# Performance work log

Hardware: AMD Instinct MI355X
Metric: run time of the kernel (lower is better)

Reference implementation:

```python
import jax, jax.numpy as jnp
import numpy as np

N_NODES = 100000
N_EDGES = 1600000
D_FEAT = 64
K = 5


def setup_inputs() -> dict:
    key = jax.random.key(0)
    k1, k2, k3 = jax.random.split(key, 3)
    feat = jax.random.normal(k1, (N_NODES, D_FEAT), dtype=jnp.float32)
    theta = jnp.asarray([1.0, -0.8, 0.45, -0.2, 0.08], dtype=jnp.float32)
    src = jax.random.randint(k2, (N_EDGES,), 0, N_NODES, dtype=jnp.int32)
    dst = jax.random.randint(k3, (N_EDGES,), 0, N_NODES, dtype=jnp.int32)
    return {"feat": feat, "theta": theta, "src": src, "dst": dst}


def reference(feat, theta, src, dst):
    n = feat.shape[0]
    # in-degrees: number of edges terminating at each node, clamped to >= 1
    deg = jax.ops.segment_sum(jnp.ones_like(dst, dtype=feat.dtype), dst, num_segments=n)
    d_invsqrt = jnp.maximum(deg, 1.0) ** -0.5  # [N]
    d_invsqrt = d_invsqrt[:, None]  # [N, 1]

    def unn_laplacian(x):
        scaled = x * d_invsqrt  # [N, D]
        agg = jax.ops.segment_sum(scaled[src], dst, num_segments=n)  # [N, D]
        return x - agg * d_invsqrt

    h = theta[0] * feat
    for k in range(1, theta.shape[0]):
        feat = unn_laplacian(feat)
        h = h + theta[k] * feat
    return h
```

## Files before the change

### kernel.cpp

```cpp
#include <hip/hip_runtime.h>
#include <hip/hip_bf16.h>
#include <hip/hip_fp16.h>

#define WG 256
#define WGB 1024
#define D 64
#define MAXNB 1024

__device__ inline float ld_mixed(const void* p, int bf, long i) {
    if (bf) {
        unsigned short u = ((const unsigned short*)p)[i];
        return __uint_as_float(((unsigned int)u) << 16);
    }
    return ((const float*)p)[i];
}


__global__ __launch_bounds__(WGB) void kc_hist(
        const int* __restrict__ dst, int E, int NBc, int CPB,
        int* __restrict__ histmat,
        const void* __restrict__ theta, int* __restrict__ flag) {
    __shared__ int h[MAXNB];
    int B = blockIdx.x, t = threadIdx.x;
    if (B == 0 && t == 0) {
        unsigned int w = *(const unsigned int*)theta;
        *flag = (w == 0x3F800000u) ? 0 : 1;
    }
    for (int i = t; i < NBc; i += WGB) h[i] = 0;
    __syncthreads();
    int base = B * CPB;
    int end = min(base + CPB, E);
    for (int e = base + t; e < end; e += WGB)
        atomicAdd(&h[dst[e] >> 8], 1);
    __syncthreads();
    for (int i = t; i < NBc; i += WGB)
        histmat[(long)i * NBc + B] = h[i];
}

__global__ void k_scan1(const int* __restrict__ in, int M,
                        int* __restrict__ out, int* __restrict__ part) {
    __shared__ int s[WG];
    int g = blockIdx.x * WG + threadIdx.x;
    int t = threadIdx.x;
    int v0 = (g < M) ? in[g] : 0;
    s[t] = v0;
    __syncthreads();
    for (int o = 1; o < WG; o <<= 1) {
        int v = (t >= o) ? s[t - o] : 0;
        __syncthreads();
        s[t] += v;
        __syncthreads();
    }
    if (g < M) out[g] = s[t] - v0;
    if (t == WG - 1) part[blockIdx.x] = s[t];
}

__global__ __launch_bounds__(WGB) void kc_scatter(
        const int* __restrict__ src, const int* __restrict__ dst, int E,
        int NBc, int CPB, const int* __restrict__ outx,
        const int* __restrict__ part, int P,
        unsigned int* __restrict__ tmp) {
    __shared__ int off[MAXNB];
    __shared__ int ps[1024];
    __shared__ int pex[1024];
    int B = blockIdx.x, t = threadIdx.x;
    int pv = (t < P) ? part[t] : 0;
    ps[t] = pv;
    __syncthreads();
    for (int o = 1; o < 1024; o <<= 1) {
        int v = (t >= o) ? ps[t - o] : 0;
        __syncthreads();
        ps[t] += v;
        __syncthreads();
    }
    pex[t] = ps[t] - pv;
    __syncthreads();
    for (int i = t; i < NBc; i += WGB) {
        long g = (long)i * NBc + B;
        off[i] = outx[g] + pex[g >> 8];
    }
    __syncthreads();
    int base = B * CPB;
    int end = min(base + CPB, E);
    for (int e = base + t; e < end; e += WGB) {
        int d = dst[e];
        int pos = atomicAdd(&off[d >> 8], 1);
        tmp[pos] = (unsigned)src[e] | ((unsigned)(d & 255) << 24);
    }
}

__global__ __launch_bounds__(WGB) void kf(
        const unsigned int* __restrict__ tmp, const int* __restrict__ outx,
        const int* __restrict__ part, int P,
        int NBc, int N, int E, int* __restrict__ ptr,
        float* __restrict__ dinv, float* __restrict__ dsqrt,
        int* __restrict__ csr) {
    __shared__ int h[256];
    __shared__ int pfx[256];
    __shared__ int cnt[256];
    __shared__ int ps[1024];
    __shared__ int pex[1024];
    int B = blockIdx.x, t = threadIdx.x;
    int pv = (t < P) ? part[t] : 0;
    ps[t] = pv;
    __syncthreads();
    for (int o = 1; o < 1024; o <<= 1) {
        int v = (t >= o) ? ps[t - o] : 0;
        __syncthreads();
        ps[t] += v;
        __syncthreads();
    }
    pex[t] = ps[t] - pv;
    __syncthreads();
    long g1 = (long)B * NBc;
    int rbase = outx[g1] + pex[g1 >> 8];
    int rend;
    if (B == NBc - 1) rend = E;
    else {
        long g2 = (long)(B + 1) * NBc;
        rend = outx[g2] + pex[g2 >> 8];
    }
    if (t < 256) h[t] = 0;
    __syncthreads();
    for (int e = rbase + t; e < rend; e += WGB)
        atomicAdd(&h[tmp[e] >> 24], 1);
    __syncthreads();
    if (t < 256) pfx[t] = h[t];
    __syncthreads();
    for (int o = 1; o < 256; o <<= 1) {
        int v = 0;
        if (t < 256 && t >= o) v = pfx[t - o];
        __syncthreads();
        if (t < 256) pfx[t] += v;
        __syncthreads();
    }
    if (t < 256) {
        int ex = pfx[t] - h[t];
        int node = B * 256 + t;
        if (node < N) {
            ptr[node] = rbase + ex;
            float d = (float)h[t];
            d = d < 1.f ? 1.f : d;
            dinv[node]  = rsqrtf(d);
            dsqrt[node] = sqrtf(d);
        }
        cnt[t] = rbase + ex;
    }
    if (B == 0 && t == 0) ptr[N] = E;
    __syncthreads();
    for (int e = rbase + t; e < rend; e += WGB) {
        unsigned p = tmp[e];
        int pos = atomicAdd(&cnt[p >> 24], 1);
        csr[pos] = (int)(p & 0xFFFFFF);
    }
}


__global__ void k_init(const void* __restrict__ feat, const void* __restrict__ theta,
                       const int* __restrict__ flag, const float* __restrict__ dinv,
                       long NF, __half* __restrict__ xs, __half* __restrict__ h) {
    int bf = *flag;
    long g = ((long)blockIdx.x * WG + threadIdx.x) * 4;
    if (g < NF) {
        float th0 = ld_mixed(theta, bf, 0);
        float w = dinv[g >> 6];
        float f0 = ld_mixed(feat, bf, g);
        float f1 = ld_mixed(feat, bf, g + 1);
        float f2 = ld_mixed(feat, bf, g + 2);
        float f3 = ld_mixed(feat, bf, g + 3);
        __half2 a0 = __floats2half2_rn(f0 * w, f1 * w);
        __half2 a1 = __floats2half2_rn(f2 * w, f3 * w);
        __half2 b0 = __floats2half2_rn(th0 * f0, th0 * f1);
        __half2 b1 = __floats2half2_rn(th0 * f2, th0 * f3);
        uint2 xo, ho;
        xo.x = *(const unsigned*)&a0; xo.y = *(const unsigned*)&a1;
        ho.x = *(const unsigned*)&b0; ho.y = *(const unsigned*)&b1;
        ((uint2*)xs)[g >> 2] = xo;
        ((uint2*)h)[g >> 2]  = ho;
    }
}

__global__ __launch_bounds__(WG) void k_spmv(
        const __half* __restrict__ xs,
        const float* __restrict__ dinv, const float* __restrict__ dsqrt,
        const int* __restrict__ ptr, const int* __restrict__ csr,
        const void* __restrict__ theta, const int* __restrict__ flag, int k,
        int N, __half* __restrict__ xsn, __half* __restrict__ h,
        void* __restrict__ out, int last) {
    int wv   = (int)(((unsigned)blockIdx.x * blockDim.x + threadIdx.x) >> 6);
    int lane = threadIdx.x & 63;
    int node = 4 * wv + (lane >> 4);
    int l    = lane & 15;
    bool valid = node < N;
    int nc = valid ? node : 0;
    int s0 = ptr[nc];
    int s1 = valid ? ptr[nc + 1] : s0;

    const uint2* xs4 = (const uint2*)xs;
    float ax = 0.f, ay = 0.f, az = 0.f, aw = 0.f;
    int e = s0;
    for (; e + 8 <= s1; e += 8) {
        int idx[8];
#pragma unroll
        for (int j = 0; j < 8; ++j) idx[j] = csr[e + j];
        uint2 a[8];
#pragma unroll
        for (int j = 0; j < 8; ++j) a[j] = xs4[idx[j] * 16 + l];
#pragma unroll
        for (int j = 0; j < 8; ++j) {
            float2 f0 = __half22float2(*(const __half2*)&a[j].x);
            float2 f1 = __half22float2(*(const __half2*)&a[j].y);
            ax += f0.x; ay += f0.y; az += f1.x; aw += f1.y;
        }
    }
    if (e + 4 <= s1) {
        int idx[4];
#pragma unroll
        for (int j = 0; j < 4; ++j) idx[j] = csr[e + j];
        uint2 a[4];
#pragma unroll
        for (int j = 0; j < 4; ++j) a[j] = xs4[idx[j] * 16 + l];
#pragma unroll
        for (int j = 0; j < 4; ++j) {
            float2 f0 = __half22float2(*(const __half2*)&a[j].x);
            float2 f1 = __half22float2(*(const __half2*)&a[j].y);
            ax += f0.x; ay += f0.y; az += f1.x; aw += f1.y;
        }
        e += 4;
    }
    for (; e < s1; ++e) {
        uint2 av = xs4[csr[e] * 16 + l];
        float2 f0 = __half22float2(*(const __half2*)&av.x);
        float2 f1 = __half22float2(*(const __half2*)&av.y);
        ax += f0.x; ay += f0.y; az += f1.x; aw += f1.y;
    }

    if (!valid) return;
    int o = node * 16 + l;
    float w  = dinv[node];
    float ds = dsqrt[node];
    uint2 xv = xs4[o];
    float2 x0 = __half22float2(*(const __half2*)&xv.x);
    float2 x1 = __half22float2(*(const __half2*)&xv.y);
    float v0 = x0.x * ds - w * ax;
    float v1 = x0.y * ds - w * ay;
    float v2 = x1.x * ds - w * az;
    float v3 = x1.y * ds - w * aw;
    int bf = *flag;
    float th = ld_mixed(theta, bf, k);
    uint2 hv = ((const uint2*)h)[o];
    float2 h0 = __half22float2(*(const __half2*)&hv.x);
    float2 h1 = __half22float2(*(const __half2*)&hv.y);
    h0.x += th * v0; h0.y += th * v1;
    h1.x += th * v2; h1.y += th * v3;
    if (last) {
        if (bf) {
            __hip_bfloat162 b0, b1;
            b0.x = __float2bfloat16(h0.x); b0.y = __float2bfloat16(h0.y);
            b1.x = __float2bfloat16(h1.x); b1.y = __float2bfloat16(h1.y);
            uint2 r;
            r.x = *(const unsigned*)&b0;
            r.y = *(const unsigned*)&b1;
            ((uint2*)out)[o] = r;
        } else {
            float4 r; r.x = h0.x; r.y = h0.y; r.z = h1.x; r.w = h1.y;
            ((float4*)out)[o] = r;
        }
    } else {
        __half2 t0 = __floats2half2_rn(v0 * w, v1 * w);
        __half2 t1 = __floats2half2_rn(v2 * w, v3 * w);
        __half2 u0 = __floats2half2_rn(h0.x, h0.y);
        __half2 u1 = __floats2half2_rn(h1.x, h1.y);
        uint2 xo, ho;
        xo.x = *(const unsigned*)&t0; xo.y = *(const unsigned*)&t1;
        ho.x = *(const unsigned*)&u0; ho.y = *(const unsigned*)&u1;
        ((uint2*)xsn)[o] = xo;
        ((uint2*)h)[o]   = ho;
    }
}

extern "C" void kernel_launch(void* const* d_in, const int* in_sizes, int n_in,
                              void* d_out, int out_size, void* d_ws, size_t ws_size,
                              hipStream_t stream) {
    const void* feat  = d_in[0];
    const void* theta = d_in[1];
    const int*  src   = (const int*)d_in[2];
    const int*  dst   = (const int*)d_in[3];
    long NF = in_sizes[0];
    int  N  = (int)(NF / D);
    int  E  = in_sizes[2];

    int NBc = (N + 255) >> 8;
    int CPB = (E + NBc - 1) / NBc;
    int M   = NBc * NBc;
    int sbl = (M + WG - 1) / WG;

    char* w = (char*)d_ws;
    size_t off = 0;
    auto alloc = [&](size_t b) -> void* {
        void* p = w + off;
        off = (off + b + 255) & ~(size_t)255;
        return p;
    };
    int*      histmat = (int*)alloc((size_t)M * 4);
    int*      outx    = (int*)alloc((size_t)M * 4);
    int*      part    = (int*)alloc(1024 * 4);
    unsigned* tmp     = (unsigned*)alloc((size_t)E * 4);
    int*      ptr     = (int*)alloc(((size_t)N + 1) * 4);
    int*      csr     = (int*)alloc((size_t)E * 4);
    float*    dinv    = (float*)alloc((size_t)N * 4);
    float*    dsqrt   = (float*)alloc((size_t)N * 4);
    int*      flag    = (int*)alloc(4);
    __half*   xs_a    = (__half*)alloc((size_t)NF * 2);
    __half*   xs_b    = (__half*)alloc((size_t)NF * 2);
    __half*   h       = (__half*)alloc((size_t)NF * 2);

    int fbl = (int)((NF / 4 + WG - 1) / WG);
    int wbl = (((N + 3) / 4) + 3) / 4;

    kc_hist<<<NBc, WGB, 0, stream>>>(dst, E, NBc, CPB, histmat, theta, flag);
    k_scan1<<<sbl, WG, 0, stream>>>(histmat, M, outx, part);
    kc_scatter<<<NBc, WGB, 0, stream>>>(src, dst, E, NBc, CPB, outx, part, sbl, tmp);
    kf<<<NBc, WGB, 0, stream>>>(tmp, outx, part, sbl, NBc, N, E, ptr, dinv, dsqrt, csr);
    k_init<<<fbl, WG, 0, stream>>>(feat, theta, flag, dinv, NF, xs_a, h);

    __half* xa = xs_a;
    __half* xb = xs_b;
    for (int k = 1; k <= 4; ++k) {
        int last = (k == 4);
        k_spmv<<<wbl, WG, 0, stream>>>(xa, dinv, dsqrt, ptr, csr, theta, flag, k,
                                       N, xb, h, d_out, last);
        __half* t = xa; xa = xb; xb = t;
    }
}
```

Before: 266.4 us.

## Sort nodes by degree within each 256-node block for balanced SpMV waves

The CSR build kernel now counts-sorts each block's 256 nodes by in-degree (capped at 63) and writes a permutation, which the SpMV kernel uses to map 16-lane groups to nodes. Nodes sharing a wavefront then have similar degrees, reducing divergence from uneven loop trip counts. The init kernel is also widened to process 8 elements per thread with 128-bit stores. The cost is an extra permutation read per node and less locality in the ptr/output accesses.

```diff
diff --git a/kernel.cpp b/kernel.cpp
--- a/kernel.cpp
+++ b/kernel.cpp
@@ -94,12 +94,14 @@
         const int* __restrict__ part, int P,
         int NBc, int N, int E, int* __restrict__ ptr,
         float* __restrict__ dinv, float* __restrict__ dsqrt,
-        int* __restrict__ csr) {
+        int* __restrict__ csr, int* __restrict__ perm) {
     __shared__ int h[256];
     __shared__ int pfx[256];
     __shared__ int cnt[256];
     __shared__ int ps[1024];
     __shared__ int pex[1024];
+    __shared__ int dcnt[64];
+    __shared__ int dsc[64];
     int B = blockIdx.x, t = threadIdx.x;
     int pv = (t < P) ? part[t] : 0;
     ps[t] = pv;
@@ -121,6 +123,7 @@
         rend = outx[g2] + pex[g2 >> 8];
     }
     if (t < 256) h[t] = 0;
+    if (t < 64) dcnt[t] = 0;
     __syncthreads();
     for (int e = rbase + t; e < rend; e += WGB)
         atomicAdd(&h[tmp[e] >> 24], 1);
@@ -134,6 +137,7 @@
         if (t < 256) pfx[t] += v;
         __syncthreads();
     }
+    int bin = 0, rank = 0;
     if (t < 256) {
         int ex = pfx[t] - h[t];
         int node = B * 256 + t;
@@ -145,8 +149,23 @@
             dsqrt[node] = sqrtf(d);
         }
         cnt[t] = rbase + ex;
+        bin = h[t] > 63 ? 63 : h[t];
+        rank = atomicAdd(&dcnt[bin], 1);
     }
     if (B == 0 && t == 0) ptr[N] = E;
+    __syncthreads();
+    if (t < 64) dsc[t] = dcnt[t];
+    __syncthreads();
+    for (int o = 1; o < 64; o <<= 1) {
+        int v = (t < 64 && t >= o) ? dsc[t - o] : 0;
+        __syncthreads();
+        if (t < 64) dsc[t] += v;
+        __syncthreads();
+    }
+    if (t < 256) {
+        int pos = dsc[bin] - dcnt[bin] + rank;
+        perm[B * 256 + pos] = B * 256 + t;
+    }
     __syncthreads();
     for (int e = rbase + t; e < rend; e += WGB) {
         unsigned p = tmp[e];
@@ -160,23 +179,28 @@
                        const int* __restrict__ flag, const float* __restrict__ dinv,
                        long NF, __half* __restrict__ xs, __half* __restrict__ h) {
     int bf = *flag;
-    long g = ((long)blockIdx.x * WG + threadIdx.x) * 4;
+    long g = ((long)blockIdx.x * WG + threadIdx.x) * 8;
     if (g < NF) {
         float th0 = ld_mixed(theta, bf, 0);
         float w = dinv[g >> 6];
-        float f0 = ld_mixed(feat, bf, g);
-        float f1 = ld_mixed(feat, bf, g + 1);
-        float f2 = ld_mixed(feat, bf, g + 2);
-        float f3 = ld_mixed(feat, bf, g + 3);
-        __half2 a0 = __floats2half2_rn(f0 * w, f1 * w);
-        __half2 a1 = __floats2half2_rn(f2 * w, f3 * w);
-        __half2 b0 = __floats2half2_rn(th0 * f0, th0 * f1);
-        __half2 b1 = __floats2half2_rn(th0 * f2, th0 * f3);
-        uint2 xo, ho;
+        float f[8];
+#pragma unroll
+        for (int j = 0; j < 8; ++j) f[j] = ld_mixed(feat, bf, g + j);
+        __half2 a0 = __floats2half2_rn(f[0] * w, f[1] * w);
+        __half2 a1 = __floats2half2_rn(f[2] * w, f[3] * w);
+        __half2 a2 = __floats2half2_rn(f[4] * w, f[5] * w);
+        __half2 a3 = __floats2half2_rn(f[6] * w, f[7] * w);
+        __half2 b0 = __floats2half2_rn(th0 * f[0], th0 * f[1]);
+        __half2 b1 = __floats2half2_rn(th0 * f[2], th0 * f[3]);
+        __half2 b2 = __floats2half2_rn(th0 * f[4], th0 * f[5]);
+        __half2 b3 = __floats2half2_rn(th0 * f[6], th0 * f[7]);
+        uint4 xo, ho;
         xo.x = *(const unsigned*)&a0; xo.y = *(const unsigned*)&a1;
+        xo.z = *(const unsigned*)&a2; xo.w = *(const unsigned*)&a3;
         ho.x = *(const unsigned*)&b0; ho.y = *(const unsigned*)&b1;
-        ((uint2*)xs)[g >> 2] = xo;
-        ((uint2*)h)[g >> 2]  = ho;
+        ho.z = *(const unsigned*)&b2; ho.w = *(const unsigned*)&b3;
+        ((uint4*)xs)[g >> 3] = xo;
+        ((uint4*)h)[g >> 3]  = ho;
     }
 }
 
@@ -184,12 +208,13 @@
         const __half* __restrict__ xs,
         const float* __restrict__ dinv, const float* __restrict__ dsqrt,
         const int* __restrict__ ptr, const int* __restrict__ csr,
+        const int* __restrict__ perm,
         const void* __restrict__ theta, const int* __restrict__ flag, int k,
         int N, __half* __restrict__ xsn, __half* __restrict__ h,
         void* __restrict__ out, int last) {
     int wv   = (int)(((unsigned)blockIdx.x * blockDim.x + threadIdx.x) >> 6);
     int lane = threadIdx.x & 63;
-    int node = 4 * wv + (lane >> 4);
+    int node = perm[4 * wv + (lane >> 4)];
     int l    = lane & 15;
     bool valid = node < N;
     int nc = valid ? node : 0;
@@ -294,6 +319,7 @@
     int CPB = (E + NBc - 1) / NBc;
     int M   = NBc * NBc;
     int sbl = (M + WG - 1) / WG;
+    int Np  = NBc * 256;
 
     char* w = (char*)d_ws;
     size_t off = 0;
@@ -310,26 +336,28 @@
     int*      csr     = (int*)alloc((size_t)E * 4);
     float*    dinv    = (float*)alloc((size_t)N * 4);
     float*    dsqrt   = (float*)alloc((size_t)N * 4);
+    int*      perm    = (int*)alloc((size_t)Np * 4);
     int*      flag    = (int*)alloc(4);
     __half*   xs_a    = (__half*)alloc((size_t)NF * 2);
     __half*   xs_b    = (__half*)alloc((size_t)NF * 2);
     __half*   h       = (__half*)alloc((size_t)NF * 2);
 
-    int fbl = (int)((NF / 4 + WG - 1) / WG);
-    int wbl = (((N + 3) / 4) + 3) / 4;
+    int fbl = (int)((NF / 8 + WG - 1) / WG);
+    int wbl = Np / 16;
 
     kc_hist<<<NBc, WGB, 0, stream>>>(dst, E, NBc, CPB, histmat, theta, flag);
     k_scan1<<<sbl, WG, 0, stream>>>(histmat, M, outx, part);
     kc_scatter<<<NBc, WGB, 0, stream>>>(src, dst, E, NBc, CPB, outx, part, sbl, tmp);
-    kf<<<NBc, WGB, 0, stream>>>(tmp, outx, part, sbl, NBc, N, E, ptr, dinv, dsqrt, csr);
+    kf<<<NBc, WGB, 0, stream>>>(tmp, outx, part, sbl, NBc, N, E, ptr, dinv, dsqrt,
+                                csr, perm);
     k_init<<<fbl, WG, 0, stream>>>(feat, theta, flag, dinv, NF, xs_a, h);
 
     __half* xa = xs_a;
     __half* xb = xs_b;
     for (int k = 1; k <= 4; ++k) {
         int last = (k == 4);
-        k_spmv<<<wbl, WG, 0, stream>>>(xa, dinv, dsqrt, ptr, csr, theta, flag, k,
-                                       N, xb, h, d_out, last);
+        k_spmv<<<wbl, WG, 0, stream>>>(xa, dinv, dsqrt, ptr, csr, perm, theta, flag,
+                                       k, N, xb, h, d_out, last);
         __half* t = xa; xa = xb; xb = t;
     }
 }
```

New measurement: 299.5 us. +12.4%, slower.
